# Optimization experiments

Measured on AMD Instinct MI355X. Metric: run time of the kernel, lower is better.

## Reference

```python
import jax, jax.numpy as jnp
import numpy as np

B, T, S, C = 16, 2048, 512, 192
NEG = -1e9  # large-negative stand-in for float32.min (avoids overflow when accumulated)


def setup_inputs() -> dict:
    key = jax.random.key(0)
    ks = jax.random.split(key, 6)
    m_p = jax.random.normal(ks[0], (B, S, C), jnp.float32)
    logs_p = jax.random.normal(ks[1], (B, S, C), jnp.float32) * 0.1
    z_p = jax.random.normal(ks[2], (B, T, C), jnp.float32)
    logs_q = jax.random.normal(ks[3], (B, T, C), jnp.float32) * 0.1
    textlen = jax.random.randint(ks[4], (B,), S // 2, S + 1, jnp.int32)
    mellen = jax.random.randint(ks[5], (B,), T // 2, T + 1, jnp.int32)
    return dict(m_p=m_p, logs_p=logs_p, z_p=z_p, logs_q=logs_q,
                textlen=textlen, mellen=mellen)


def monotonic_alignment_search(ll, textlen, mellen):
    """Viterbi-style monotonic alignment. ll: [B, T, S] -> attn [B, T, S]."""
    Bb, Tt, Ss = ll.shape
    s_range = jnp.arange(Ss)
    ll_t = jnp.transpose(ll, (1, 0, 2))  # [T, B, S]

    def fwd(prob, xt):
        t, ll_row = xt
        prev = jnp.concatenate([jnp.full((Bb, 1), NEG, ll.dtype), prob[:, :-1]], axis=1)
        stay = prob >= prev  # True: best path stays at same text index
        prob = jnp.where(s_range[None] <= t, jnp.maximum(prob, prev) + ll_row, NEG)
        return prob, stay

    _, direction = jax.lax.scan(fwd, jnp.zeros((Bb, Ss), ll.dtype),
                                (jnp.arange(Tt), ll_t))  # direction: [T, B, S] bool

    def bwd(idx, xt):
        t, dir_t = xt
        active = t < mellen  # [B]
        onehot = (s_range[None] == idx[:, None]) & active[:, None]  # [B, S]
        stay = jnp.take_along_axis(dir_t, idx[:, None], axis=1)[:, 0]
        new_idx = jnp.where(active, idx - (1 - stay.astype(jnp.int32)), idx)
        return new_idx, onehot

    _, attn_rev = jax.lax.scan(bwd, textlen - 1,
                               (jnp.arange(Tt - 1, -1, -1), direction[::-1]))
    attn = attn_rev[::-1].astype(ll.dtype)  # [T, B, S]
    return jnp.transpose(attn, (1, 0, 2))


def reference(m_p, logs_p, z_p, logs_q, textlen, mellen):
    tmask = (jnp.arange(S)[None] < textlen[:, None]).astype(jnp.float32)  # [B, S]
    mmask = (jnp.arange(T)[None] < mellen[:, None]).astype(jnp.float32)   # [B, T]
    attnmask = mmask[:, :, None] * tmask[:, None]                          # [B, T, S]

    # Negative cross-entropy score matrix [B, T, S]
    s_sq_r = jnp.exp(-2.0 * logs_p)  # [B, S, C]
    nc1 = jnp.sum(-0.5 * np.log(2.0 * np.pi) - logs_p, axis=-1)[:, None]  # [B, 1, S]
    nc2 = jnp.einsum('btc,bsc->bts', -0.5 * z_p ** 2, s_sq_r)
    nc3 = jnp.einsum('btc,bsc->bts', z_p, m_p * s_sq_r)
    nc4 = jnp.sum(-0.5 * m_p ** 2 * s_sq_r, axis=-1)[:, None]             # [B, 1, S]
    neg_cent = nc1 + nc2 + nc3 + nc4

    ll = jnp.where(attnmask > 0, neg_cent, NEG)
    attn = jax.lax.stop_gradient(monotonic_alignment_search(ll, textlen, mellen))

    # Expand text-level stats to frame level via the hard alignment
    m_e = jnp.einsum('bts,bsc->btc', attn, m_p)
    l_e = jnp.einsum('bts,bsc->btc', attn, logs_p)

    kl = l_e - logs_q - 0.5 + 0.5 * (z_p - m_e) ** 2 * jnp.exp(-2.0 * l_e)
    kl = jnp.sum(kl * mmask[..., None]) / jnp.sum(mmask)
    return kl, attn
```

## Files before the change

kernel.cpp:

```cpp
#include <hip/hip_runtime.h>

#define NEGV (-1e9f)

static const int B_ = 16;
static const int T_ = 2048;
static const int S_ = 512;
static const int C_ = 192;

typedef unsigned short ushort_t;
using f32x4 = __attribute__((ext_vector_type(4))) float;
using s16x8 = __attribute__((ext_vector_type(8))) short;

__device__ __forceinline__ void split2(float x, ushort_t& h, ushort_t& l) {
    __bf16 hb = (__bf16)x;
    h = __builtin_bit_cast(ushort_t, hb);
    float r = x - (float)hb;
    __bf16 lb = (__bf16)r;
    l = __builtin_bit_cast(ushort_t, lb);
}

__device__ __forceinline__ ushort_t to_bf16(float x) {
    return __builtin_bit_cast(ushort_t, (__bf16)x);
}

__global__ __launch_bounds__(256)
void prep_kernel(const float* __restrict__ m_p, const float* __restrict__ logs_p,
                 ushort_t* __restrict__ Bh, ushort_t* __restrict__ Bl,
                 float* __restrict__ nc14) {
    int wid = (blockIdx.x * blockDim.x + threadIdx.x) >> 6;
    int lane = threadIdx.x & 63;
    if (wid >= B_ * S_) return;
    const float HALF_LOG_2PI = 0.9189385332046727f;
    const float* mrow = m_p    + (size_t)wid * C_;
    const float* lrow = logs_p + (size_t)wid * C_;
    ushort_t* bh = Bh + (size_t)wid * 384;
    ushort_t* bl = Bl + (size_t)wid * 384;
    float tot = 0.f;
#pragma unroll
    for (int q = 0; q < 3; ++q) {
        int c = lane + q * 64;
        float m  = mrow[c];
        float lp = lrow[c];
        float s2r = __expf(-2.f * lp);
        float a = m * s2r;
        ushort_t h, l;
        split2(a, h, l);   bh[c] = h;        bl[c] = l;
        split2(s2r, h, l); bh[192 + c] = h;  bl[192 + c] = l;
        tot += (-HALF_LOG_2PI - lp) + (-0.5f * m * m * s2r);
    }
#pragma unroll
    for (int off = 32; off > 0; off >>= 1) tot += __shfl_xor(tot, off);
    if (lane == 0) nc14[wid] = tot;
}

#define LDP 40
__global__ __launch_bounds__(256)
void gemm_kernel(const float* __restrict__ z_p,
                 const ushort_t* __restrict__ Bh, const ushort_t* __restrict__ Bl,
                 const float* __restrict__ nc14,
                 const int* __restrict__ textlen, const int* __restrict__ mellen,
                 float* __restrict__ ll) {
    __shared__ ushort_t sAh[128 * LDP];
    __shared__ ushort_t sBh[128 * LDP];
    __shared__ ushort_t sBl[128 * LDP];

    const int b  = blockIdx.z;
    const int t0 = blockIdx.y * 128;
    const int s0 = blockIdx.x * 128;
    const int tid = threadIdx.x;
    const int lane = tid & 63;
    const int wave = tid >> 6;
    const int wr = wave >> 1, wc = wave & 1;
    const int srow = tid >> 1;
    const int cb = (tid & 1) * 16;

    const int ml = mellen[b], tl = textlen[b];
    const int r15 = lane & 15;
    const int klane = (lane >> 4) * 8;

    if (t0 >= ml || s0 >= tl) {
        int scol[4];
#pragma unroll
        for (int n = 0; n < 4; ++n) scol[n] = s0 + wc * 64 + n * 16 + r15;
#pragma unroll
        for (int m = 0; m < 4; ++m) {
            const int tb = t0 + wr * 64 + m * 16 + (lane >> 4) * 4;
#pragma unroll
            for (int r = 0; r < 4; ++r) {
                float* orow = ll + ((size_t)b * T_ + tb + r) * S_;
#pragma unroll
                for (int n = 0; n < 4; ++n) orow[scol[n]] = NEGV;
            }
        }
        return;
    }

    f32x4 acc[4][4];
#pragma unroll
    for (int m = 0; m < 4; ++m)
#pragma unroll
        for (int n = 0; n < 4; ++n) acc[m][n] = (f32x4){0.f, 0.f, 0.f, 0.f};

    for (int kk = 0; kk < 12; ++kk) {
        {
            const int ck = (kk < 6 ? kk * 32 : (kk - 6) * 32) + cb;
            const float* src = z_p + ((size_t)b * T_ + t0 + srow) * C_ + ck;
            float e[16];
            *(float4*)(e + 0)  = *(const float4*)(src + 0);
            *(float4*)(e + 4)  = *(const float4*)(src + 4);
            *(float4*)(e + 8)  = *(const float4*)(src + 8);
            *(float4*)(e + 12) = *(const float4*)(src + 12);
            if (kk >= 6) {
#pragma unroll
                for (int i = 0; i < 16; ++i) e[i] = -0.5f * e[i] * e[i];
            }
            ushort_t h[16];
#pragma unroll
            for (int i = 0; i < 16; ++i) h[i] = to_bf16(e[i]);
            ushort_t* dh = &sAh[srow * LDP + cb];
            *(uint4*)dh = make_uint4(h[0] | (h[1] << 16), h[2] | (h[3] << 16),
                                     h[4] | (h[5] << 16), h[6] | (h[7] << 16));
            *(uint4*)(dh + 8) = make_uint4(h[8] | (h[9] << 16), h[10] | (h[11] << 16),
                                           h[12] | (h[13] << 16), h[14] | (h[15] << 16));
        }
        {
            const size_t off = ((size_t)b * S_ + s0 + srow) * 384 + kk * 32 + cb;
            const uint4 u0 = *(const uint4*)(Bh + off);
            const uint4 u1 = *(const uint4*)(Bh + off + 8);
            const uint4 v0 = *(const uint4*)(Bl + off);
            const uint4 v1 = *(const uint4*)(Bl + off + 8);
            ushort_t* dh = &sBh[srow * LDP + cb];
            ushort_t* dl = &sBl[srow * LDP + cb];
            *(uint4*)dh = u0; *(uint4*)(dh + 8) = u1;
            *(uint4*)dl = v0; *(uint4*)(dl + 8) = v1;
        }
        __syncthreads();

        s16x8 ah[4], bhf[4], blf[4];
#pragma unroll
        for (int m = 0; m < 4; ++m) {
            const int row = wr * 64 + m * 16 + r15;
            ah[m] = *(const s16x8*)&sAh[row * LDP + klane];
        }
#pragma unroll
        for (int n = 0; n < 4; ++n) {
            const int row = wc * 64 + n * 16 + r15;
            bhf[n] = *(const s16x8*)&sBh[row * LDP + klane];
            blf[n] = *(const s16x8*)&sBl[row * LDP + klane];
        }
#pragma unroll
        for (int m = 0; m < 4; ++m)
#pragma unroll
            for (int n = 0; n < 4; ++n) {
                acc[m][n] = __builtin_amdgcn_mfma_f32_16x16x32_bf16(ah[m], bhf[n], acc[m][n], 0, 0, 0);
                acc[m][n] = __builtin_amdgcn_mfma_f32_16x16x32_bf16(ah[m], blf[n], acc[m][n], 0, 0, 0);
            }
        __syncthreads();
    }

    int scol[4]; float ncv[4];
#pragma unroll
    for (int n = 0; n < 4; ++n) {
        scol[n] = s0 + wc * 64 + n * 16 + r15;
        ncv[n] = nc14[b * S_ + scol[n]];
    }
#pragma unroll
    for (int m = 0; m < 4; ++m) {
        const int tb = t0 + wr * 64 + m * 16 + (lane >> 4) * 4;
#pragma unroll
        for (int r = 0; r < 4; ++r) {
            const int t = tb + r;
            const bool tm = (t < ml);
            float* orow = ll + ((size_t)b * T_ + t) * S_;
#pragma unroll
            for (int n = 0; n < 4; ++n)
                orow[scol[n]] = (tm && scol[n] < tl) ? (acc[m][n][r] + ncv[n]) : NEGV;
        }
    }
}

__global__ __launch_bounds__(64)
void mas_forward(const float* __restrict__ ll, unsigned char* __restrict__ dir) {
    const int b = blockIdx.x;
    const int lane = threadIdx.x;
    const float* llb = ll + (size_t)b * T_ * S_ + lane * 8;
    unsigned char* db = dir + ((size_t)b * T_) * 64 + lane;
    const int sbase = lane * 8;

    float4 pre[8][2];
#pragma unroll
    for (int r = 0; r < 8; ++r) {
        pre[r][0] = *(const float4*)(llb + (size_t)r * S_);
        pre[r][1] = *(const float4*)(llb + (size_t)r * S_ + 4);
    }

    float p[8];
#pragma unroll
    for (int j = 0; j < 8; ++j) p[j] = 0.f;
    float carry = (lane == 0) ? NEGV : 0.f;

    auto step = [&](int t, int ph, bool masked) {
        float cur[8];
        cur[0] = pre[ph][0].x; cur[1] = pre[ph][0].y;
        cur[2] = pre[ph][0].z; cur[3] = pre[ph][0].w;
        cur[4] = pre[ph][1].x; cur[5] = pre[ph][1].y;
        cur[6] = pre[ph][1].z; cur[7] = pre[ph][1].w;
        const int tn = t + 8;
        if (tn < T_) {
            pre[ph][0] = *(const float4*)(llb + (size_t)tn * S_);
            pre[ph][1] = *(const float4*)(llb + (size_t)tn * S_ + 4);
        }
        float v7 = fmaxf(p[7], p[6]) + cur[7];
        float nc7 = masked ? ((sbase + 7 <= t) ? v7 : NEGV) : v7;
        float newcarry = __shfl_up(nc7, 1);

        unsigned bits = (p[0] >= carry) ? 1u : 0u;
#pragma unroll
        for (int j = 1; j < 8; ++j)
            bits |= (p[j] >= p[j - 1] ? 1u : 0u) << j;

        float nv[8];
        nv[0] = fmaxf(p[0], carry) + cur[0];
#pragma unroll
        for (int j = 1; j < 7; ++j) nv[j] = fmaxf(p[j], p[j - 1]) + cur[j];
        nv[7] = v7;
        if (masked) {
#pragma unroll
            for (int j = 0; j < 8; ++j)
                p[j] = (sbase + j <= t) ? nv[j] : NEGV;
        } else {
#pragma unroll
            for (int j = 0; j < 8; ++j) p[j] = nv[j];
        }
        carry = (lane == 0) ? NEGV : newcarry;
        db[(size_t)t * 64] = (unsigned char)bits;
    };

    for (int to = 0; to < S_ / 8; ++to) {
#pragma unroll
        for (int ph = 0; ph < 8; ++ph) step(to * 8 + ph, ph, true);
    }
    for (int to = S_ / 8; to < T_ / 8; ++to) {
#pragma unroll
        for (int ph = 0; ph < 8; ++ph) step(to * 8 + ph, ph, false);
    }
}

__global__ __launch_bounds__(64)
void mas_backward(const unsigned char* __restrict__ dir,
                  const int* __restrict__ textlen, const int* __restrict__ mellen,
                  int* __restrict__ idx_arr) {
    const int b = blockIdx.x;
    const int lane = threadIdx.x;
    const int tl = textlen[b], ml = mellen[b];
    for (int t = ml + lane; t < T_; t += 64) idx_arr[b * T_ + t] = -1;
    const unsigned char* db = dir + (size_t)b * T_ * 64;
    int idx = tl - 1;
    int t_hi = ml - 1;

    auto loadwin = [&](int throw_, int anchor, int& base) -> unsigned {
        const int B = anchor >> 3;
        const int b0 = (B > 3) ? (B - 3) : 0;
        base = b0;
        unsigned w = 0;
        const int t = throw_ - lane;
        if (lane < 8 && t >= 0) {
            const unsigned char* p = db + (size_t)t * 64 + b0;
            w = (unsigned)p[0] | ((unsigned)p[1] << 8) |
                ((unsigned)p[2] << 16) | ((unsigned)p[3] << 24);
        }
        return w;
    };

    int b00, b01;
    unsigned w0 = loadwin(t_hi, idx, b00);
    unsigned w1 = loadwin(t_hi - 8, idx, b01);

    while (t_hi >= 0) {
        int b02;
        unsigned w2 = loadwin(t_hi - 16, idx, b02);

        unsigned vk[8];
#pragma unroll
        for (int k = 0; k < 8; ++k) vk[k] = __shfl((int)w0, k);
        int emit = -1;
#pragma unroll
        for (int k = 0; k < 8; ++k) {
            const int tt = t_hi - k;
            if (tt < 0) break;
            if (lane == k) emit = idx;
            const int off = (idx >> 3) - b00;
            const unsigned byte = (vk[k] >> (off * 8)) & 0xffu;
            const int stay = (byte >> (idx & 7)) & 1;
            idx -= (1 - stay);
            if (idx < 0) idx = 0;
        }
        const int tt = t_hi - lane;
        if (lane < 8 && tt >= 0) idx_arr[b * T_ + tt] = emit;
        w0 = w1; b00 = b01;
        w1 = w2; b01 = b02;
        t_hi -= 8;
    }
}

__global__ __launch_bounds__(256)
void attn_kl(const float* __restrict__ m_p, const float* __restrict__ logs_p,
             const float* __restrict__ z_p, const float* __restrict__ logs_q,
             const int* __restrict__ idx_arr, const int* __restrict__ mellen,
             float* __restrict__ attn, float* __restrict__ frame_kl) {
    const int wid = (blockIdx.x * blockDim.x + threadIdx.x) >> 6;
    const int lane = threadIdx.x & 63;
    if (wid >= B_ * T_) return;
    const int b = wid >> 11;
    const int t = wid & (T_ - 1);
    const int ml = mellen[b];
    const int idx = idx_arr[wid];

    float* row = attn + (size_t)wid * S_;
#pragma unroll
    for (int j = 0; j < 8; ++j) {
        const int s = j * 64 + lane;
        row[s] = (s == idx) ? 1.0f : 0.0f;
    }

    float total = 0.f;
    if (t < ml) {
        const float* mr = m_p    + ((size_t)b * S_ + idx) * C_;
        const float* lr = logs_p + ((size_t)b * S_ + idx) * C_;
        const float* zr = z_p    + (size_t)wid * C_;
        const float* qr = logs_q + (size_t)wid * C_;
#pragma unroll
        for (int q = 0; q < 3; ++q) {
            const int c = lane + q * 64;
            const float le = lr[c];
            const float d = zr[c] - mr[c];
            total += le - qr[c] - 0.5f + 0.5f * d * d * __expf(-2.f * le);
        }
    }
#pragma unroll
    for (int off = 32; off > 0; off >>= 1) total += __shfl_xor(total, off);
    if (lane == 0) frame_kl[wid] = total;
}

__global__ __launch_bounds__(256)
void kl_reduce(const float* __restrict__ frame_kl, const int* __restrict__ mellen,
               float* __restrict__ out) {
    __shared__ float sm[256];
    const int tid = threadIdx.x;
    float s = 0.f;
    for (int k = tid; k < B_ * T_; k += 256) s += frame_kl[k];
    sm[tid] = s;
    __syncthreads();
    for (int off = 128; off > 0; off >>= 1) {
        if (tid < off) sm[tid] += sm[tid + off];
        __syncthreads();
    }
    if (tid == 0) {
        int sum_ml = 0;
        for (int bq = 0; bq < B_; ++bq) sum_ml += mellen[bq];
        out[0] = sm[0] / (float)sum_ml;
    }
}

extern "C" void kernel_launch(void* const* d_in, const int* in_sizes, int n_in,
                              void* d_out, int out_size, void* d_ws, size_t ws_size,
                              hipStream_t stream) {
    const float* m_p    = (const float*)d_in[0];
    const float* logs_p = (const float*)d_in[1];
    const float* z_p    = (const float*)d_in[2];
    const float* logs_q = (const float*)d_in[3];
    const int*   textlen = (const int*)d_in[4];
    const int*   mellen  = (const int*)d_in[5];

    float* out = (float*)d_out;
    float* attn = out + 1;
    float* ll = attn;

    char* ws = (char*)d_ws;
    const size_t OFF_BH   = 0;
    const size_t OFF_BL   = OFF_BH + (size_t)B_ * S_ * 384 * 2;
    const size_t OFF_NC   = OFF_BL + (size_t)B_ * S_ * 384 * 2;
    const size_t OFF_DIR  = OFF_NC + (size_t)B_ * S_ * 4;
    const size_t OFF_IDX  = OFF_DIR + (size_t)B_ * T_ * 64;
    const size_t OFF_FKL  = OFF_IDX + (size_t)B_ * T_ * 4;
    ushort_t* Bh = (ushort_t*)(ws + OFF_BH);
    ushort_t* Bl = (ushort_t*)(ws + OFF_BL);
    float* nc14 = (float*)(ws + OFF_NC);
    unsigned char* dir = (unsigned char*)(ws + OFF_DIR);
    int* idx_arr = (int*)(ws + OFF_IDX);
    float* frame_kl = (float*)(ws + OFF_FKL);

    prep_kernel<<<(B_ * S_) / 4, 256, 0, stream>>>(m_p, logs_p, Bh, Bl, nc14);
    gemm_kernel<<<dim3(S_ / 128, T_ / 128, B_), 256, 0, stream>>>(
        z_p, Bh, Bl, nc14, textlen, mellen, ll);
    mas_forward<<<B_, 64, 0, stream>>>(ll, dir);
    mas_backward<<<B_, 64, 0, stream>>>(dir, textlen, mellen, idx_arr);
    attn_kl<<<(B_ * T_) / 4, 256, 0, stream>>>(m_p, logs_p, z_p, logs_q,
                                               idx_arr, mellen, attn, frame_kl);
    kl_reduce<<<1, 256, 0, stream>>>(frame_kl, mellen, out);
}
```

Measured before the change: 485.4 us.

## Fuse GEMM and MAS forward with per-tile flags so Viterbi overlaps GEMM

The GEMM kernel and the MAS forward scan are merged into one launch. The first 16 blocks run the per-batch Viterbi forward pass and spin on per-(batch, T-tile) atomic counters. The GEMM blocks, reordered so T-tiles go out in order, increment those counters after writing their ll tile. This lets the serial forward scan start while the GEMM is still running, hiding most of the GEMM time behind the latency-bound recurrence. It relies on the forward blocks being scheduled first and staying resident, and it reuses the idx_arr workspace as the flag array, cleared with a memset.

Measured after the change: 757.6 us. 56.1% more time.

```diff
diff --git a/kernel.cpp b/kernel.cpp
--- a/kernel.cpp
+++ b/kernel.cpp
@@ -53,20 +53,116 @@
     if (lane == 0) nc14[wid] = tot;
 }
 
+__device__ __noinline__ void mas_forward_body(const float* __restrict__ llb0,
+                                              unsigned char* __restrict__ db0,
+                                              const int* __restrict__ flags) {
+    const int lane = threadIdx.x;
+    const float* llb = llb0 + lane * 8;
+    unsigned char* db = db0 + lane;
+    const int sbase = lane * 8;
+
+    auto wait_tile = [&](int tt) {
+        while (__hip_atomic_load(&flags[tt], __ATOMIC_ACQUIRE,
+                                 __HIP_MEMORY_SCOPE_AGENT) < 4) {}
+    };
+
+    wait_tile(0);
+
+    float4 pre[8][2];
+#pragma unroll
+    for (int r = 0; r < 8; ++r) {
+        pre[r][0] = *(const float4*)(llb + (size_t)r * S_);
+        pre[r][1] = *(const float4*)(llb + (size_t)r * S_ + 4);
+    }
+
+    float p[8];
+#pragma unroll
+    for (int j = 0; j < 8; ++j) p[j] = 0.f;
+    float carry = (lane == 0) ? NEGV : 0.f;
+
+    auto step = [&](int t, int ph, bool masked) {
+        float cur[8];
+        cur[0] = pre[ph][0].x; cur[1] = pre[ph][0].y;
+        cur[2] = pre[ph][0].z; cur[3] = pre[ph][0].w;
+        cur[4] = pre[ph][1].x; cur[5] = pre[ph][1].y;
+        cur[6] = pre[ph][1].z; cur[7] = pre[ph][1].w;
+        const int tn = t + 8;
+        if (tn < T_) {
+            pre[ph][0] = *(const float4*)(llb + (size_t)tn * S_);
+            pre[ph][1] = *(const float4*)(llb + (size_t)tn * S_ + 4);
+        }
+        float v7 = fmaxf(p[7], p[6]) + cur[7];
+        float nc7 = masked ? ((sbase + 7 <= t) ? v7 : NEGV) : v7;
+        float newcarry = __shfl_up(nc7, 1);
+
+        unsigned bits = (p[0] >= carry) ? 1u : 0u;
+#pragma unroll
+        for (int j = 1; j < 8; ++j)
+            bits |= (p[j] >= p[j - 1] ? 1u : 0u) << j;
+
+        float nv[8];
+        nv[0] = fmaxf(p[0], carry) + cur[0];
+#pragma unroll
+        for (int j = 1; j < 7; ++j) nv[j] = fmaxf(p[j], p[j - 1]) + cur[j];
+        nv[7] = v7;
+        if (masked) {
+#pragma unroll
+            for (int j = 0; j < 8; ++j)
+                p[j] = (sbase + j <= t) ? nv[j] : NEGV;
+        } else {
+#pragma unroll
+            for (int j = 0; j < 8; ++j) p[j] = nv[j];
+        }
+        carry = (lane == 0) ? NEGV : newcarry;
+        db[(size_t)t * 64] = (unsigned char)bits;
+    };
+
+    for (int tt = 0; tt < 4; ++tt) {
+        wait_tile(tt + 1);
+        for (int to2 = 0; to2 < 16; ++to2) {
+            const int to = tt * 16 + to2;
+#pragma unroll
+            for (int ph = 0; ph < 8; ++ph) step(to * 8 + ph, ph, true);
+        }
+    }
+    for (int tt = 4; tt < 16; ++tt) {
+        wait_tile(tt < 15 ? tt + 1 : 15);
+        for (int to2 = 0; to2 < 16; ++to2) {
+            const int to = tt * 16 + to2;
+#pragma unroll
+            for (int ph = 0; ph < 8; ++ph) step(to * 8 + ph, ph, false);
+        }
+    }
+}
+
 #define LDP 40
 __global__ __launch_bounds__(256)
-void gemm_kernel(const float* __restrict__ z_p,
-                 const ushort_t* __restrict__ Bh, const ushort_t* __restrict__ Bl,
-                 const float* __restrict__ nc14,
-                 const int* __restrict__ textlen, const int* __restrict__ mellen,
-                 float* __restrict__ ll) {
+void fused_gemm_fwd(const float* __restrict__ z_p,
+                    const ushort_t* __restrict__ Bh, const ushort_t* __restrict__ Bl,
+                    const float* __restrict__ nc14,
+                    const int* __restrict__ textlen, const int* __restrict__ mellen,
+                    float* __restrict__ ll, unsigned char* __restrict__ dir,
+                    int* __restrict__ flags) {
     __shared__ ushort_t sAh[128 * LDP];
     __shared__ ushort_t sBh[128 * LDP];
     __shared__ ushort_t sBl[128 * LDP];
 
-    const int b  = blockIdx.z;
-    const int t0 = blockIdx.y * 128;
-    const int s0 = blockIdx.x * 128;
+    if (blockIdx.x < 16) {
+        if (threadIdx.x >= 64) return;
+        const int b = blockIdx.x;
+        mas_forward_body(ll + (size_t)b * T_ * S_,
+                         dir + (size_t)b * T_ * 64,
+                         flags + b * 16);
+        return;
+    }
+
+    const int gi = (int)blockIdx.x - 16;
+    const int t_tile = gi >> 6;
+    const int rem = gi & 63;
+    const int b = rem >> 2;
+    const int s_tile = rem & 3;
+    const int t0 = t_tile * 128;
+    const int s0 = s_tile * 128;
     const int tid = threadIdx.x;
     const int lane = tid & 63;
     const int wave = tid >> 6;
@@ -92,6 +188,11 @@
                 for (int n = 0; n < 4; ++n) orow[scol[n]] = NEGV;
             }
         }
+        __threadfence();
+        __syncthreads();
+        if (tid == 0)
+            __hip_atomic_fetch_add(&flags[b * 16 + t_tile], 1,
+                                   __ATOMIC_RELEASE, __HIP_MEMORY_SCOPE_AGENT);
         return;
     }
 
@@ -177,73 +278,11 @@
                 orow[scol[n]] = (tm && scol[n] < tl) ? (acc[m][n][r] + ncv[n]) : NEGV;
         }
     }
-}
-
-__global__ __launch_bounds__(64)
-void mas_forward(const float* __restrict__ ll, unsigned char* __restrict__ dir) {
-    const int b = blockIdx.x;
-    const int lane = threadIdx.x;
-    const float* llb = ll + (size_t)b * T_ * S_ + lane * 8;
-    unsigned char* db = dir + ((size_t)b * T_) * 64 + lane;
-    const int sbase = lane * 8;
-
-    float4 pre[8][2];
-#pragma unroll
-    for (int r = 0; r < 8; ++r) {
-        pre[r][0] = *(const float4*)(llb + (size_t)r * S_);
-        pre[r][1] = *(const float4*)(llb + (size_t)r * S_ + 4);
-    }
-
-    float p[8];
-#pragma unroll
-    for (int j = 0; j < 8; ++j) p[j] = 0.f;
-    float carry = (lane == 0) ? NEGV : 0.f;
-
-    auto step = [&](int t, int ph, bool masked) {
-        float cur[8];
-        cur[0] = pre[ph][0].x; cur[1] = pre[ph][0].y;
-        cur[2] = pre[ph][0].z; cur[3] = pre[ph][0].w;
-        cur[4] = pre[ph][1].x; cur[5] = pre[ph][1].y;
-        cur[6] = pre[ph][1].z; cur[7] = pre[ph][1].w;
-        const int tn = t + 8;
-        if (tn < T_) {
-            pre[ph][0] = *(const float4*)(llb + (size_t)tn * S_);
-            pre[ph][1] = *(const float4*)(llb + (size_t)tn * S_ + 4);
-        }
-        float v7 = fmaxf(p[7], p[6]) + cur[7];
-        float nc7 = masked ? ((sbase + 7 <= t) ? v7 : NEGV) : v7;
-        float newcarry = __shfl_up(nc7, 1);
-
-        unsigned bits = (p[0] >= carry) ? 1u : 0u;
-#pragma unroll
-        for (int j = 1; j < 8; ++j)
-            bits |= (p[j] >= p[j - 1] ? 1u : 0u) << j;
-
-        float nv[8];
-        nv[0] = fmaxf(p[0], carry) + cur[0];
-#pragma unroll
-        for (int j = 1; j < 7; ++j) nv[j] = fmaxf(p[j], p[j - 1]) + cur[j];
-        nv[7] = v7;
-        if (masked) {
-#pragma unroll
-            for (int j = 0; j < 8; ++j)
-                p[j] = (sbase + j <= t) ? nv[j] : NEGV;
-        } else {
-#pragma unroll
-            for (int j = 0; j < 8; ++j) p[j] = nv[j];
-        }
-        carry = (lane == 0) ? NEGV : newcarry;
-        db[(size_t)t * 64] = (unsigned char)bits;
-    };
-
-    for (int to = 0; to < S_ / 8; ++to) {
-#pragma unroll
-        for (int ph = 0; ph < 8; ++ph) step(to * 8 + ph, ph, true);
-    }
-    for (int to = S_ / 8; to < T_ / 8; ++to) {
-#pragma unroll
-        for (int ph = 0; ph < 8; ++ph) step(to * 8 + ph, ph, false);
-    }
+    __threadfence();
+    __syncthreads();
+    if (tid == 0)
+        __hip_atomic_fetch_add(&flags[b * 16 + t_tile], 1,
+                               __ATOMIC_RELEASE, __HIP_MEMORY_SCOPE_AGENT);
 }
 
 __global__ __launch_bounds__(64)
@@ -388,12 +427,13 @@
     float* nc14 = (float*)(ws + OFF_NC);
     unsigned char* dir = (unsigned char*)(ws + OFF_DIR);
     int* idx_arr = (int*)(ws + OFF_IDX);
+    int* flags = idx_arr;
     float* frame_kl = (float*)(ws + OFF_FKL);
 
     prep_kernel<<<(B_ * S_) / 4, 256, 0, stream>>>(m_p, logs_p, Bh, Bl, nc14);
-    gemm_kernel<<<dim3(S_ / 128, T_ / 128, B_), 256, 0, stream>>>(
-        z_p, Bh, Bl, nc14, textlen, mellen, ll);
-    mas_forward<<<B_, 64, 0, stream>>>(ll, dir);
+    hipMemsetAsync(flags, 0, 16 * 16 * sizeof(int), stream);
+    fused_gemm_fwd<<<16 + 16 * 64, 256, 0, stream>>>(
+        z_p, Bh, Bl, nc14, textlen, mellen, ll, dir, flags);
     mas_backward<<<B_, 64, 0, stream>>>(dir, textlen, mellen, idx_arr);
     attn_kl<<<(B_ * T_) / 4, 256, 0, stream>>>(m_p, logs_p, z_p, logs_q,
                                                idx_arr, mellen, attn, frame_kl);
```
